# Optimization experiments

Measured on AMD Instinct MI355X. Metric: run time of the kernel, lower is better.

## Reference

```python
import jax, jax.numpy as jnp
import numpy as np

EMB_DIM = 300
TEMPERATURE = 0.01
REWEIGHT = True
N = 8192
NUM_GROUPS = 100


def setup_inputs() -> dict:
    key = jax.random.key(0)
    ks = jax.random.split(key, 6)
    s = 1.0 / np.sqrt(EMB_DIM)
    x = jax.random.normal(ks[0], (N, EMB_DIM), dtype=jnp.float32)
    W1 = jax.random.normal(ks[1], (EMB_DIM, EMB_DIM), dtype=jnp.float32) * s
    b1 = jnp.zeros((EMB_DIM,), dtype=jnp.float32)
    W2 = jax.random.normal(ks[2], (EMB_DIM, EMB_DIM), dtype=jnp.float32) * s
    b2 = jnp.zeros((EMB_DIM,), dtype=jnp.float32)
    # labels in [1, 100]: all > 0 so the group_y>0 filter keeps every row
    labels = jax.random.randint(ks[3], (N,), 1, NUM_GROUPS + 1, dtype=jnp.int32)
    return {"x": x, "W1": W1, "b1": b1, "W2": W2, "b2": b2, "labels": labels}


def reference(x, W1, b1, W2, b2, labels):
    # projector: Linear -> ReLU -> Linear
    h = jax.nn.relu(x @ W1 + b1) @ W2 + b2
    # L2 normalize rows
    f = h / jnp.linalg.norm(h, axis=1, keepdims=True)
    # pairwise similarity / temperature, row-max subtracted (detached)
    logits = (f @ f.T) / TEMPERATURE                      # [N, N]
    logits = logits - jax.lax.stop_gradient(jnp.max(logits, axis=1, keepdims=True))

    lab = labels[:, None]
    mask = (lab == lab.T).astype(logits.dtype)            # same-group mask
    logits_mask = 1.0 - jnp.eye(mask.shape[0], dtype=logits.dtype)  # drop diagonal
    mask = mask * logits_mask

    # rows with at least one positive (torch filters these; we weight instead)
    pos_count = jnp.sum(mask, axis=1)                     # [N]
    valid = pos_count > 0

    if REWEIGHT:
        pos_m = logits_mask * mask
        neg_m = logits_mask * (1.0 - mask)
        pos_sum = jnp.sum(pos_m, axis=1, keepdims=True)
        neg_sum = jnp.sum(neg_m, axis=1, keepdims=True)
        log_pos = jnp.where(pos_sum > 0, jnp.log(jnp.maximum(pos_sum, 1.0)), 0.0)
        log_neg = jnp.where(neg_sum > 0, jnp.log(jnp.maximum(neg_sum, 1.0)), 0.0)
        logits = (logits - log_pos) * pos_m + (logits - log_neg) * neg_m

    exp_logits = jnp.exp(logits) * logits_mask
    log_prob = logits - jnp.log(jnp.sum(exp_logits, axis=1, keepdims=True))
    mean_log_prob_pos = jnp.sum(mask * log_prob, axis=1) / jnp.where(valid, pos_count, 1.0)
    validf = valid.astype(logits.dtype)
    loss = -TEMPERATURE * jnp.sum(mean_log_prob_pos * validf) / jnp.sum(validf)
    return loss
```

## Files before the change

### kernel.cpp

```cpp
#include <hip/hip_runtime.h>
#include <hip/hip_bf16.h>


#define N_ROWS 8192
#define D_PAD 320
#define NG 100
#define TEMP 0.01f
#define NSPLIT 32
#define JCHUNK (N_ROWS / NSPLIT)
#define IBLK 128
#define JTILE 32
#define LOG2E100 144.2695041f

typedef short short8v __attribute__((ext_vector_type(8)));
typedef float float4v __attribute__((ext_vector_type(4)));

__device__ __forceinline__ short f2bf(float f) {
  union { __hip_bfloat16 h; short s; } u;
  u.h = __float2bfloat16(f);
  return u.s;
}

__global__ __launch_bounds__(256) void setup_kernel(
    const float* __restrict__ W1, const float* __restrict__ W2,
    const int* __restrict__ labels,
    __hip_bfloat16* __restrict__ w1t, __hip_bfloat16* __restrict__ w2t,
    int* __restrict__ counts)
{
  __shared__ int hc[NG + 1];
  int b = blockIdx.x, tid = threadIdx.x;
  if (b < 800) {
    int isW2 = (b >= 400);
    int idx = (b - (isW2 ? 400 : 0)) * 256 + tid;
    const float* W = isW2 ? W2 : W1;
    __hip_bfloat16* dst = isW2 ? w2t : w1t;
    int n = idx / D_PAD, k = idx - n * D_PAD;
    float v = (n < 300 && k < 300) ? W[(size_t)k * 300 + n] : 0.0f;
    dst[idx] = __float2bfloat16(v);
  } else {
    if (tid <= NG) hc[tid] = 0;
    __syncthreads();
    int row = (b - 800) * 256 + tid;
    atomicAdd(&hc[labels[row]], 1);
    __syncthreads();
    if (tid <= NG && hc[tid] > 0) atomicAdd(&counts[tid], hc[tid]);
  }
}

__global__ __launch_bounds__(256, 2) void mlp_fused_kernel(
    const float* __restrict__ x, const __hip_bfloat16* __restrict__ w1t,
    const __hip_bfloat16* __restrict__ w2t, const float* __restrict__ b1,
    const float* __restrict__ b2, __hip_bfloat16* __restrict__ fb)
{
  __shared__ __align__(16) short Ws[64 * D_PAD];
  __shared__ __align__(16) short H1[64 * D_PAD];
  int tid = threadIdx.x;
  int lane = tid & 63, wave = tid >> 6;
  int g = lane >> 4, lc = lane & 15, sw = lc & 7;
  int i0 = blockIdx.x * 64;

  short8v afr[10];
  {
    const float* xp = x + (size_t)(i0 + wave * 16 + lc) * 300;
#pragma unroll
    for (int kk = 0; kk < 10; ++kk) {
      int k0 = kk * 32 + g * 8;
      short8v v;
      if (k0 + 8 <= 300) {
        float4 a = *(const float4*)(xp + k0);
        float4 c = *(const float4*)(xp + k0 + 4);
        v[0] = f2bf(a.x); v[1] = f2bf(a.y); v[2] = f2bf(a.z); v[3] = f2bf(a.w);
        v[4] = f2bf(c.x); v[5] = f2bf(c.y); v[6] = f2bf(c.z); v[7] = f2bf(c.w);
      } else if (k0 < 300) {
        float4 a = *(const float4*)(xp + k0);
        v[0] = f2bf(a.x); v[1] = f2bf(a.y); v[2] = f2bf(a.z); v[3] = f2bf(a.w);
        v[4] = 0; v[5] = 0; v[6] = 0; v[7] = 0;
      } else {
        v = short8v{0, 0, 0, 0, 0, 0, 0, 0};
      }
      afr[kk] = v;
    }
  }

  for (int c = 0; c < 5; ++c) {
    __syncthreads();
    {
      const int4* src = (const int4*)w1t;
      int4* dst = (int4*)Ws;
#pragma unroll
      for (int t = 0; t < 10; ++t) {
        int e = tid + t * 256;
        int r = e / 40, q = e - r * 40;
        dst[r * 40 + (q ^ (r & 7))] = src[(size_t)(c * 64 + r) * 40 + q];
      }
    }
    __syncthreads();
    for (int js = 0; js < 4; ++js) {
      float4v acc = {0.f, 0.f, 0.f, 0.f};
      const short* rowp = Ws + (js * 16 + lc) * D_PAD;
#pragma unroll
      for (int kk = 0; kk < 10; ++kk) {
        short8v bf = *(const short8v*)(rowp + (((g + 4 * kk) ^ sw) << 3));
        acc = __builtin_amdgcn_mfma_f32_16x16x32_bf16(afr[kk], bf, acc, 0, 0, 0);
      }
      int n = c * 64 + js * 16 + lc;
      float bv = (n < 300) ? b1[n] : 0.0f;
#pragma unroll
      for (int r = 0; r < 4; ++r) {
        int row = wave * 16 + g * 4 + r;
        int q = n >> 3;
        H1[row * D_PAD + ((q ^ (row & 7)) << 3) + (n & 7)] =
            f2bf(fmaxf(acc[r] + bv, 0.0f));
      }
    }
  }
  __syncthreads();

  short8v hfr[10];
  {
    const short* rp = H1 + (wave * 16 + lc) * D_PAD;
#pragma unroll
    for (int kk = 0; kk < 10; ++kk)
      hfr[kk] = *(const short8v*)(rp + (((g + 4 * kk) ^ sw) << 3));
  }

  float4v h2a[5][4];
  for (int c = 0; c < 5; ++c) {
    __syncthreads();
    {
      const int4* src = (const int4*)w2t;
      int4* dst = (int4*)Ws;
#pragma unroll
      for (int t = 0; t < 10; ++t) {
        int e = tid + t * 256;
        int r = e / 40, q = e - r * 40;
        dst[r * 40 + (q ^ (r & 7))] = src[(size_t)(c * 64 + r) * 40 + q];
      }
    }
    __syncthreads();
#pragma unroll
    for (int js = 0; js < 4; ++js) {
      float4v acc = {0.f, 0.f, 0.f, 0.f};
      const short* rowp = Ws + (js * 16 + lc) * D_PAD;
#pragma unroll
      for (int kk = 0; kk < 10; ++kk) {
        short8v bf = *(const short8v*)(rowp + (((g + 4 * kk) ^ sw) << 3));
        acc = __builtin_amdgcn_mfma_f32_16x16x32_bf16(hfr[kk], bf, acc, 0, 0, 0);
      }
      int n = c * 64 + js * 16 + lc;
      float bv = (n < 300) ? b2[n] : 0.0f;
#pragma unroll
      for (int r = 0; r < 4; ++r) acc[r] += bv;
      h2a[c][js] = acc;
    }
  }

  float ssq[4] = {0.f, 0.f, 0.f, 0.f};
#pragma unroll
  for (int c = 0; c < 5; ++c)
#pragma unroll
    for (int js = 0; js < 4; ++js)
#pragma unroll
      for (int r = 0; r < 4; ++r) ssq[r] = fmaf(h2a[c][js][r], h2a[c][js][r], ssq[r]);
  for (int m = 1; m < 16; m <<= 1)
#pragma unroll
    for (int r = 0; r < 4; ++r) ssq[r] += __shfl_xor(ssq[r], m, 64);
  float inv[4];
#pragma unroll
  for (int r = 0; r < 4; ++r) inv[r] = rsqrtf(ssq[r]);
#pragma unroll
  for (int c = 0; c < 5; ++c)
#pragma unroll
    for (int js = 0; js < 4; ++js) {
      int n = c * 64 + js * 16 + lc;
#pragma unroll
      for (int r = 0; r < 4; ++r) {
        int row = i0 + wave * 16 + g * 4 + r;
        fb[(size_t)row * D_PAD + n] = __float2bfloat16(h2a[c][js][r] * inv[r]);
      }
    }
}

__global__ __launch_bounds__(256) void group_kernel(
    const __hip_bfloat16* __restrict__ Fb, const int* __restrict__ labels,
    float* __restrict__ sPar, float* __restrict__ sAar)
{
  __shared__ __align__(16) short Bs[64 * D_PAD];
  __shared__ int memb[256];
  __shared__ int cnt;
  const short* Fs = (const short*)Fb;
  int tid = threadIdx.x;
  int lane = tid & 63, wave = tid >> 6;
  int g = lane >> 4, lc = lane & 15, sw = lc & 7;
  int grp = blockIdx.x + 1;
  if (tid == 0) cnt = 0;
  __syncthreads();
  for (int i = tid; i < N_ROWS; i += 256)
    if (labels[i] == grp) { int p = atomicAdd(&cnt, 1); if (p < 256) memb[p] = i; }
  __syncthreads();
  int c = cnt > 256 ? 256 : cnt;
  int nt = (c + 63) >> 6;
  for (int it = 0; it < nt; ++it) {
    short8v afr[10];
    {
      int islot = it * 64 + wave * 16 + lc;
      int arow = memb[islot < c ? islot : 0];
      const short* ap = Fs + (size_t)arow * D_PAD + g * 8;
#pragma unroll
      for (int kk = 0; kk < 10; ++kk) afr[kk] = *(const short8v*)(ap + kk * 32);
    }
    int iglobr[4]; bool ivalid[4];
    for (int r = 0; r < 4; ++r) {
      int islot = it * 64 + wave * 16 + g * 4 + r;
      ivalid[r] = islot < c;
      iglobr[r] = memb[islot < c ? islot : 0];
    }
    float sp[4] = {}, sa[4] = {};
    for (int jt = 0; jt < nt; ++jt) {
      __syncthreads();
      {
        const int4* src = (const int4*)Fs;
        int4* dst = (int4*)Bs;
#pragma unroll
        for (int t = 0; t < 10; ++t) {
          int e = tid + t * 256;
          int r = e / 40, q = e - r * 40;
          int jslot = jt * 64 + r;
          int grow = memb[jslot < c ? jslot : 0];
          dst[r * 40 + (q ^ (r & 7))] = src[(size_t)grow * 40 + q];
        }
      }
      __syncthreads();
      for (int js = 0; js < 4; ++js) {
        float4v acc = {0.f, 0.f, 0.f, 0.f};
        const short* rowp = Bs + (js * 16 + lc) * D_PAD;
#pragma unroll
        for (int kk = 0; kk < 10; ++kk) {
          short8v bf = *(const short8v*)(rowp + (((g + 4 * kk) ^ sw) << 3));
          acc = __builtin_amdgcn_mfma_f32_16x16x32_bf16(afr[kk], bf, acc, 0, 0, 0);
        }
        int jslot = jt * 64 + js * 16 + lc;
        bool jv = jslot < c;
        int jglob = memb[jslot < c ? jslot : 0];
#pragma unroll
        for (int r = 0; r < 4; ++r) {
          float a = acc[r];
          float e = exp2f(fmaf(a, LOG2E100, -LOG2E100));
          bool ok = jv && ivalid[r] && (jglob != iglobr[r]);
          sp[r] += ok ? e : 0.f;
          sa[r] += ok ? a : 0.f;
        }
      }
    }
    for (int m = 1; m < 16; m <<= 1)
      for (int r = 0; r < 4; ++r) {
        sp[r] += __shfl_xor(sp[r], m, 64);
        sa[r] += __shfl_xor(sa[r], m, 64);
      }
    if (lc == 0)
      for (int r = 0; r < 4; ++r)
        if (ivalid[r]) { sPar[iglobr[r]] = sp[r]; sAar[iglobr[r]] = sa[r]; }
  }
}

__device__ __forceinline__ void stage_tile32(const short* __restrict__ Fs, int jb,
                                             short* __restrict__ buf, int tid)
{
  int lane = tid & 63;
  int wbase = tid - lane;
#pragma unroll
  for (int t = 0; t < 5; ++t) {
    int ebase = t * 256 + wbase;
    int e = ebase + lane;
    int r = e / 40, qs = e - r * 40;
    int q = qs ^ (r & 7);
    const int4* gsrc = (const int4*)(Fs + (size_t)(jb + r) * D_PAD) + q;
    __builtin_amdgcn_global_load_lds(
        (const __attribute__((address_space(1))) void*)gsrc,
        (__attribute__((address_space(3))) void*)((int4*)buf + ebase),
        16, 0, 0);
  }
}

__global__ __launch_bounds__(256, 2) void pairwise_kernel(
    const __hip_bfloat16* __restrict__ Fb, float* __restrict__ partE)
{
  __shared__ __align__(16) short Bs[2][JTILE * D_PAD];
  const short* Fs = (const short*)Fb;
  int tid = threadIdx.x;
  int lane = tid & 63, wave = tid >> 6;
  int g = lane >> 4, lc = lane & 15, sw = lc & 7;
  int i0 = blockIdx.x * IBLK;
  int split = blockIdx.y;
  int jstart = split * JCHUNK;

  short8v afr[2][10];
#pragma unroll
  for (int s = 0; s < 2; ++s) {
    const short* ap = Fs + (size_t)(i0 + s * 64 + wave * 16 + lc) * D_PAD + g * 8;
#pragma unroll
    for (int kk = 0; kk < 10; ++kk) afr[s][kk] = *(const short8v*)(ap + kk * 32);
  }
  float sE[2][4] = {};

  stage_tile32(Fs, jstart, &Bs[0][0], tid);
  __syncthreads();

  for (int jt = 0; jt < JCHUNK / JTILE; ++jt) {
    int jb = jstart + jt * JTILE;
    int cur = jt & 1;
    if (jt + 1 < JCHUNK / JTILE)
      stage_tile32(Fs, jb + JTILE, &Bs[cur ^ 1][0], tid);

    const short* bufp = &Bs[cur][0];
    for (int js = 0; js < JTILE / 16; ++js) {
      float4v acc0 = {0.f, 0.f, 0.f, 0.f}, acc1 = {0.f, 0.f, 0.f, 0.f};
      const short* rowp = bufp + (js * 16 + lc) * D_PAD;
#pragma unroll
      for (int kk = 0; kk < 10; ++kk) {
        short8v bf = *(const short8v*)(rowp + (((g + 4 * kk) ^ sw) << 3));
        acc0 = __builtin_amdgcn_mfma_f32_16x16x32_bf16(afr[0][kk], bf, acc0, 0, 0, 0);
        acc1 = __builtin_amdgcn_mfma_f32_16x16x32_bf16(afr[1][kk], bf, acc1, 0, 0, 0);
      }
      int jgrp = jb + js * 16;
#pragma unroll
      for (int s = 0; s < 2; ++s) {
        float4v acc = s ? acc1 : acc0;
        bool dtile = (jgrp == i0 + s * 64 + wave * 16);
#pragma unroll
        for (int r = 0; r < 4; ++r) {
          float e = exp2f(fmaf(acc[r], LOG2E100, -LOG2E100));
          if (dtile && lc == g * 4 + r) e = 0.0f;
          sE[s][r] += e;
        }
      }
    }
    __syncthreads();
  }

  for (int m = 1; m < 16; m <<= 1)
#pragma unroll
    for (int s = 0; s < 2; ++s)
#pragma unroll
      for (int r = 0; r < 4; ++r) sE[s][r] += __shfl_xor(sE[s][r], m, 64);
  if (lc == 0)
#pragma unroll
    for (int s = 0; s < 2; ++s)
#pragma unroll
      for (int r = 0; r < 4; ++r)
        partE[split * N_ROWS + i0 + s * 64 + wave * 16 + g * 4 + r] = sE[s][r];
}

__global__ __launch_bounds__(256) void final_a_kernel(
    const float* __restrict__ partE, const float* __restrict__ sPar,
    const float* __restrict__ sAar, const int* __restrict__ counts,
    const int* __restrict__ labels, float* __restrict__ blk)
{
  int tid = threadIdx.x;
  int i = blockIdx.x * 256 + tid;
  float sE = 0.f;
  for (int s = 0; s < NSPLIT; ++s) sE += partE[s * N_ROWS + i];
  float M = 0.f, V = 0.f;
  int pc = counts[labels[i]] - 1;
  if (pc > 0) {
    float P = sPar[i], A = sAar[i];
    float Q = sE - P;
    float pcf = (float)pc, ncf = (float)(N_ROWS - 1 - pc);
    float Z = P / pcf + Q / ncf;
    M = 100.0f * A / pcf - 100.0f - logf(pcf) - logf(Z);
    V = 1.f;
  }
  __shared__ float rm[256], rv[256];
  rm[tid] = M; rv[tid] = V;
  __syncthreads();
  for (int s2 = 128; s2 > 0; s2 >>= 1) {
    if (tid < s2) { rm[tid] += rm[tid + s2]; rv[tid] += rv[tid + s2]; }
    __syncthreads();
  }
  if (tid == 0) { blk[blockIdx.x] = rm[0]; blk[32 + blockIdx.x] = rv[0]; }
}

__global__ void final_b_kernel(const float* __restrict__ blk, float* __restrict__ out)
{
  int lane = threadIdx.x;
  float m = (lane < 32) ? blk[lane] : 0.f;
  float v = (lane < 32) ? blk[32 + lane] : 0.f;
  for (int s = 1; s < 32; s <<= 1) { m += __shfl_xor(m, s, 64); v += __shfl_xor(v, s, 64); }
  if (lane == 0) out[0] = (v > 0.f) ? (-TEMP * m / v) : 0.f;
}

extern "C" void kernel_launch(void* const* d_in, const int* in_sizes, int n_in,
                              void* d_out, int out_size, void* d_ws, size_t ws_size,
                              hipStream_t stream)
{
  const float* x  = (const float*)d_in[0];
  const float* W1 = (const float*)d_in[1];
  const float* b1 = (const float*)d_in[2];
  const float* W2 = (const float*)d_in[3];
  const float* b2 = (const float*)d_in[4];
  const int* labels = (const int*)d_in[5];

  char* ws = (char*)d_ws;
  __hip_bfloat16* fb  = (__hip_bfloat16*)(ws);
  __hip_bfloat16* w1t = (__hip_bfloat16*)(ws + 5242880);
  __hip_bfloat16* w2t = (__hip_bfloat16*)(ws + 5447680);
  int*         counts = (int*)(ws + 5652480);
  float*        partE = (float*)(ws + 5652992);
  float*        sPar  = (float*)(ws + 6701568);
  float*        sAar  = (float*)(ws + 6734336);
  float*        blk   = (float*)(ws + 6767104);

  hipMemsetAsync(counts, 0, (NG + 1) * sizeof(int), stream);
  setup_kernel<<<832, 256, 0, stream>>>(W1, W2, labels, w1t, w2t, counts);
  mlp_fused_kernel<<<N_ROWS / 64, 256, 0, stream>>>(x, w1t, w2t, b1, b2, fb);
  group_kernel<<<NG, 256, 0, stream>>>(fb, labels, sPar, sAar);
  pairwise_kernel<<<dim3(N_ROWS / IBLK, NSPLIT), 256, 0, stream>>>(fb, partE);
  final_a_kernel<<<32, 256, 0, stream>>>(partE, sPar, sAar, counts, labels, blk);
  final_b_kernel<<<1, 64, 0, stream>>>(blk, (float*)d_out);
}
```

Measured before the change: 169.4 us.

## Merge group and pairwise kernels, fuse final reductions, drop memset and counts pass

Folds the per-group positive-pair kernel into the pairwise kernel as extra leading blocks, so the group work overlaps with the pairwise tiles in a single launch. The two final reduction kernels become one, using an atomic ticket so the last block produces the scalar loss. The label histogram moves from the setup kernel into each final block, which removes the memset and the atomics from setup. This cuts launch count and serialization gaps, at the cost of each final block rescanning all labels and some workspace aliasing: blk overlays the w1t buffer and the ticket sits just after it.

```diff
diff --git a/kernel.cpp b/kernel.cpp
--- a/kernel.cpp
+++ b/kernel.cpp
@@ -23,28 +23,16 @@
 
 __global__ __launch_bounds__(256) void setup_kernel(
     const float* __restrict__ W1, const float* __restrict__ W2,
-    const int* __restrict__ labels,
-    __hip_bfloat16* __restrict__ w1t, __hip_bfloat16* __restrict__ w2t,
-    int* __restrict__ counts)
-{
-  __shared__ int hc[NG + 1];
+    __hip_bfloat16* __restrict__ w1t, __hip_bfloat16* __restrict__ w2t)
+{
   int b = blockIdx.x, tid = threadIdx.x;
-  if (b < 800) {
-    int isW2 = (b >= 400);
-    int idx = (b - (isW2 ? 400 : 0)) * 256 + tid;
-    const float* W = isW2 ? W2 : W1;
-    __hip_bfloat16* dst = isW2 ? w2t : w1t;
-    int n = idx / D_PAD, k = idx - n * D_PAD;
-    float v = (n < 300 && k < 300) ? W[(size_t)k * 300 + n] : 0.0f;
-    dst[idx] = __float2bfloat16(v);
-  } else {
-    if (tid <= NG) hc[tid] = 0;
-    __syncthreads();
-    int row = (b - 800) * 256 + tid;
-    atomicAdd(&hc[labels[row]], 1);
-    __syncthreads();
-    if (tid <= NG && hc[tid] > 0) atomicAdd(&counts[tid], hc[tid]);
-  }
+  int isW2 = (b >= 400);
+  int idx = (b - (isW2 ? 400 : 0)) * 256 + tid;
+  const float* W = isW2 ? W2 : W1;
+  __hip_bfloat16* dst = isW2 ? w2t : w1t;
+  int n = idx / D_PAD, k = idx - n * D_PAD;
+  float v = (n < 300 && k < 300) ? W[(size_t)k * 300 + n] : 0.0f;
+  dst[idx] = __float2bfloat16(v);
 }
 
 __global__ __launch_bounds__(256, 2) void mlp_fused_kernel(
@@ -181,87 +169,6 @@
     }
 }
 
-__global__ __launch_bounds__(256) void group_kernel(
-    const __hip_bfloat16* __restrict__ Fb, const int* __restrict__ labels,
-    float* __restrict__ sPar, float* __restrict__ sAar)
-{
-  __shared__ __align__(16) short Bs[64 * D_PAD];
-  __shared__ int memb[256];
-  __shared__ int cnt;
-  const short* Fs = (const short*)Fb;
-  int tid = threadIdx.x;
-  int lane = tid & 63, wave = tid >> 6;
-  int g = lane >> 4, lc = lane & 15, sw = lc & 7;
-  int grp = blockIdx.x + 1;
-  if (tid == 0) cnt = 0;
-  __syncthreads();
-  for (int i = tid; i < N_ROWS; i += 256)
-    if (labels[i] == grp) { int p = atomicAdd(&cnt, 1); if (p < 256) memb[p] = i; }
-  __syncthreads();
-  int c = cnt > 256 ? 256 : cnt;
-  int nt = (c + 63) >> 6;
-  for (int it = 0; it < nt; ++it) {
-    short8v afr[10];
-    {
-      int islot = it * 64 + wave * 16 + lc;
-      int arow = memb[islot < c ? islot : 0];
-      const short* ap = Fs + (size_t)arow * D_PAD + g * 8;
-#pragma unroll
-      for (int kk = 0; kk < 10; ++kk) afr[kk] = *(const short8v*)(ap + kk * 32);
-    }
-    int iglobr[4]; bool ivalid[4];
-    for (int r = 0; r < 4; ++r) {
-      int islot = it * 64 + wave * 16 + g * 4 + r;
-      ivalid[r] = islot < c;
-      iglobr[r] = memb[islot < c ? islot : 0];
-    }
-    float sp[4] = {}, sa[4] = {};
-    for (int jt = 0; jt < nt; ++jt) {
-      __syncthreads();
-      {
-        const int4* src = (const int4*)Fs;
-        int4* dst = (int4*)Bs;
-#pragma unroll
-        for (int t = 0; t < 10; ++t) {
-          int e = tid + t * 256;
-          int r = e / 40, q = e - r * 40;
-          int jslot = jt * 64 + r;
-          int grow = memb[jslot < c ? jslot : 0];
-          dst[r * 40 + (q ^ (r & 7))] = src[(size_t)grow * 40 + q];
-        }
-      }
-      __syncthreads();
-      for (int js = 0; js < 4; ++js) {
-        float4v acc = {0.f, 0.f, 0.f, 0.f};
-        const short* rowp = Bs + (js * 16 + lc) * D_PAD;
-#pragma unroll
-        for (int kk = 0; kk < 10; ++kk) {
-          short8v bf = *(const short8v*)(rowp + (((g + 4 * kk) ^ sw) << 3));
-          acc = __builtin_amdgcn_mfma_f32_16x16x32_bf16(afr[kk], bf, acc, 0, 0, 0);
-        }
-        int jslot = jt * 64 + js * 16 + lc;
-        bool jv = jslot < c;
-        int jglob = memb[jslot < c ? jslot : 0];
-#pragma unroll
-        for (int r = 0; r < 4; ++r) {
-          float a = acc[r];
-          float e = exp2f(fmaf(a, LOG2E100, -LOG2E100));
-          bool ok = jv && ivalid[r] && (jglob != iglobr[r]);
-          sp[r] += ok ? e : 0.f;
-          sa[r] += ok ? a : 0.f;
-        }
-      }
-    }
-    for (int m = 1; m < 16; m <<= 1)
-      for (int r = 0; r < 4; ++r) {
-        sp[r] += __shfl_xor(sp[r], m, 64);
-        sa[r] += __shfl_xor(sa[r], m, 64);
-      }
-    if (lc == 0)
-      for (int r = 0; r < 4; ++r)
-        if (ivalid[r]) { sPar[iglobr[r]] = sp[r]; sAar[iglobr[r]] = sa[r]; }
-  }
-}
 
 __device__ __forceinline__ void stage_tile32(const short* __restrict__ Fs, int jb,
                                              short* __restrict__ buf, int tid)
@@ -282,16 +189,99 @@
   }
 }
 
-__global__ __launch_bounds__(256, 2) void pairwise_kernel(
-    const __hip_bfloat16* __restrict__ Fb, float* __restrict__ partE)
+__global__ __launch_bounds__(256, 2) void pairgroup_kernel(
+    const __hip_bfloat16* __restrict__ Fb, const int* __restrict__ labels,
+    float* __restrict__ partE, float* __restrict__ sPar,
+    float* __restrict__ sAar, int* __restrict__ ticket)
 {
   __shared__ __align__(16) short Bs[2][JTILE * D_PAD];
+  __shared__ int memb[256];
+  __shared__ int cnt;
   const short* Fs = (const short*)Fb;
   int tid = threadIdx.x;
   int lane = tid & 63, wave = tid >> 6;
   int g = lane >> 4, lc = lane & 15, sw = lc & 7;
-  int i0 = blockIdx.x * IBLK;
-  int split = blockIdx.y;
+  int bx = blockIdx.x;
+
+  if (bx == 0 && tid == 0) atomicExch(ticket, 0);
+
+  if (bx < NG) {
+    short* Bsf = &Bs[0][0];
+    int grp = bx + 1;
+    if (tid == 0) cnt = 0;
+    __syncthreads();
+    for (int i = tid; i < N_ROWS; i += 256)
+      if (labels[i] == grp) { int p = atomicAdd(&cnt, 1); if (p < 256) memb[p] = i; }
+    __syncthreads();
+    int c = cnt > 256 ? 256 : cnt;
+    int nt = (c + 63) >> 6;
+    for (int it = 0; it < nt; ++it) {
+      short8v afr[10];
+      {
+        int islot = it * 64 + wave * 16 + lc;
+        int arow = memb[islot < c ? islot : 0];
+        const short* ap = Fs + (size_t)arow * D_PAD + g * 8;
+#pragma unroll
+        for (int kk = 0; kk < 10; ++kk) afr[kk] = *(const short8v*)(ap + kk * 32);
+      }
+      int iglobr[4]; bool ivalid[4];
+      for (int r = 0; r < 4; ++r) {
+        int islot = it * 64 + wave * 16 + g * 4 + r;
+        ivalid[r] = islot < c;
+        iglobr[r] = memb[islot < c ? islot : 0];
+      }
+      float sp[4] = {}, sa[4] = {};
+      for (int jt = 0; jt < nt; ++jt) {
+        __syncthreads();
+        {
+          const int4* src = (const int4*)Fs;
+          int4* dst = (int4*)Bsf;
+#pragma unroll
+          for (int t = 0; t < 10; ++t) {
+            int e = tid + t * 256;
+            int r = e / 40, q = e - r * 40;
+            int jslot = jt * 64 + r;
+            int grow = memb[jslot < c ? jslot : 0];
+            dst[r * 40 + (q ^ (r & 7))] = src[(size_t)grow * 40 + q];
+          }
+        }
+        __syncthreads();
+        for (int js = 0; js < 4; ++js) {
+          float4v acc = {0.f, 0.f, 0.f, 0.f};
+          const short* rowp = Bsf + (js * 16 + lc) * D_PAD;
+#pragma unroll
+          for (int kk = 0; kk < 10; ++kk) {
+            short8v bf = *(const short8v*)(rowp + (((g + 4 * kk) ^ sw) << 3));
+            acc = __builtin_amdgcn_mfma_f32_16x16x32_bf16(afr[kk], bf, acc, 0, 0, 0);
+          }
+          int jslot = jt * 64 + js * 16 + lc;
+          bool jv = jslot < c;
+          int jglob = memb[jslot < c ? jslot : 0];
+#pragma unroll
+          for (int r = 0; r < 4; ++r) {
+            float a = acc[r];
+            float e = exp2f(fmaf(a, LOG2E100, -LOG2E100));
+            bool ok = jv && ivalid[r] && (jglob != iglobr[r]);
+            sp[r] += ok ? e : 0.f;
+            sa[r] += ok ? a : 0.f;
+          }
+        }
+      }
+      for (int m = 1; m < 16; m <<= 1)
+        for (int r = 0; r < 4; ++r) {
+          sp[r] += __shfl_xor(sp[r], m, 64);
+          sa[r] += __shfl_xor(sa[r], m, 64);
+        }
+      if (lc == 0)
+        for (int r = 0; r < 4; ++r)
+          if (ivalid[r]) { sPar[iglobr[r]] = sp[r]; sAar[iglobr[r]] = sa[r]; }
+    }
+    return;
+  }
+
+  int pb = bx - NG;
+  int i0 = (pb & 63) * IBLK;
+  int split = pb >> 6;
   int jstart = split * JCHUNK;
 
   short8v afr[2][10];
@@ -351,17 +341,25 @@
         partE[split * N_ROWS + i0 + s * 64 + wave * 16 + g * 4 + r] = sE[s][r];
 }
 
-__global__ __launch_bounds__(256) void final_a_kernel(
+__global__ __launch_bounds__(256) void final_kernel(
     const float* __restrict__ partE, const float* __restrict__ sPar,
-    const float* __restrict__ sAar, const int* __restrict__ counts,
-    const int* __restrict__ labels, float* __restrict__ blk)
-{
+    const float* __restrict__ sAar, const int* __restrict__ labels,
+    float* __restrict__ blk, int* __restrict__ ticket, float* __restrict__ out)
+{
+  __shared__ int hc[NG + 1];
+  __shared__ float rm[256], rv[256];
+  __shared__ int winner;
   int tid = threadIdx.x;
+  if (tid <= NG) hc[tid] = 0;
+  __syncthreads();
+  for (int i2 = tid; i2 < N_ROWS; i2 += 256) atomicAdd(&hc[labels[i2]], 1);
+  __syncthreads();
+
   int i = blockIdx.x * 256 + tid;
   float sE = 0.f;
   for (int s = 0; s < NSPLIT; ++s) sE += partE[s * N_ROWS + i];
   float M = 0.f, V = 0.f;
-  int pc = counts[labels[i]] - 1;
+  int pc = hc[labels[i]] - 1;
   if (pc > 0) {
     float P = sPar[i], A = sAar[i];
     float Q = sE - P;
@@ -370,23 +368,29 @@
     M = 100.0f * A / pcf - 100.0f - logf(pcf) - logf(Z);
     V = 1.f;
   }
-  __shared__ float rm[256], rv[256];
   rm[tid] = M; rv[tid] = V;
   __syncthreads();
   for (int s2 = 128; s2 > 0; s2 >>= 1) {
     if (tid < s2) { rm[tid] += rm[tid + s2]; rv[tid] += rv[tid + s2]; }
     __syncthreads();
   }
-  if (tid == 0) { blk[blockIdx.x] = rm[0]; blk[32 + blockIdx.x] = rv[0]; }
-}
-
-__global__ void final_b_kernel(const float* __restrict__ blk, float* __restrict__ out)
-{
-  int lane = threadIdx.x;
-  float m = (lane < 32) ? blk[lane] : 0.f;
-  float v = (lane < 32) ? blk[32 + lane] : 0.f;
-  for (int s = 1; s < 32; s <<= 1) { m += __shfl_xor(m, s, 64); v += __shfl_xor(v, s, 64); }
-  if (lane == 0) out[0] = (v > 0.f) ? (-TEMP * m / v) : 0.f;
+  if (tid == 0) {
+    blk[blockIdx.x * 16] = rm[0];
+    blk[(32 + blockIdx.x) * 16] = rv[0];
+    __threadfence();
+    int old = atomicAdd(ticket, 1);
+    winner = (old == 31);
+  }
+  __syncthreads();
+  if (winner && tid < 64) {
+    float m = (tid < 32) ? atomicAdd(&blk[tid * 16], 0.0f) : 0.f;
+    float v = (tid < 32) ? atomicAdd(&blk[(32 + tid) * 16], 0.0f) : 0.f;
+    for (int s = 1; s < 32; s <<= 1) {
+      m += __shfl_xor(m, s, 64);
+      v += __shfl_xor(v, s, 64);
+    }
+    if (tid == 0) out[0] = (v > 0.f) ? (-TEMP * m / v) : 0.f;
+  }
 }
 
 extern "C" void kernel_launch(void* const* d_in, const int* in_sizes, int n_in,
@@ -404,17 +408,16 @@
   __hip_bfloat16* fb  = (__hip_bfloat16*)(ws);
   __hip_bfloat16* w1t = (__hip_bfloat16*)(ws + 5242880);
   __hip_bfloat16* w2t = (__hip_bfloat16*)(ws + 5447680);
-  int*         counts = (int*)(ws + 5652480);
-  float*        partE = (float*)(ws + 5652992);
-  float*        sPar  = (float*)(ws + 6701568);
-  float*        sAar  = (float*)(ws + 6734336);
-  float*        blk   = (float*)(ws + 6767104);
-
-  hipMemsetAsync(counts, 0, (NG + 1) * sizeof(int), stream);
-  setup_kernel<<<832, 256, 0, stream>>>(W1, W2, labels, w1t, w2t, counts);
+  float*        partE = (float*)(ws + 5652480);
+  float*        sPar  = (float*)(ws + 6701056);
+  float*        sAar  = (float*)(ws + 6733824);
+  float*        blk   = (float*)(ws + 5242880);
+  int*          ticket= (int*)(ws + 5242880 + 4096);
+
+  setup_kernel<<<800, 256, 0, stream>>>(W1, W2, w1t, w2t);
   mlp_fused_kernel<<<N_ROWS / 64, 256, 0, stream>>>(x, w1t, w2t, b1, b2, fb);
-  group_kernel<<<NG, 256, 0, stream>>>(fb, labels, sPar, sAar);
-  pairwise_kernel<<<dim3(N_ROWS / IBLK, NSPLIT), 256, 0, stream>>>(fb, partE);
-  final_a_kernel<<<32, 256, 0, stream>>>(partE, sPar, sAar, counts, labels, blk);
-  final_b_kernel<<<1, 64, 0, stream>>>(blk, (float*)d_out);
-}
+  pairgroup_kernel<<<NG + (N_ROWS / IBLK) * NSPLIT, 256, 0, stream>>>(
+      fb, labels, partE, sPar, sAar, ticket);
+  final_kernel<<<32, 256, 0, stream>>>(partE, sPar, sAar, labels, blk, ticket,
+                                       (float*)d_out);
+}
```

After: 161.2 us. 4.9% less time.
